# Kernel tuning notes

Measured on AMD Instinct MI355X. Metric: run time of the kernel, lower is better.

Reference implementation:

```python
import jax, jax.numpy as jnp
import numpy as np

B, DIN, E, FACTOR, STEPS, NH = 2048, 1024, 1024, 16, 3, 8
DH = E // NH
EPS = 1e-5


def layernorm(x, g, b):
    m = x.mean(-1, keepdims=True)
    v = ((x - m) ** 2).mean(-1, keepdims=True)
    return (x - m) / jnp.sqrt(v + EPS) * g + b


def setup_inputs() -> dict:
    key = jax.random.key(0)
    ks = iter(jax.random.split(key, 32))
    r = lambda shape, s=0.02: jax.random.normal(next(ks), shape, dtype=jnp.float32) * s
    F = E * FACTOR
    return {
        "image_feat": jax.random.normal(next(ks), (B, DIN), dtype=jnp.float32),
        "text_feat": jax.random.normal(next(ks), (B, DIN), dtype=jnp.float32),
        # fusion block
        "fc1_w": r((F, DIN)), "fc1_b": jnp.zeros((F,), jnp.float32),
        "fc2_w": r((F, DIN)), "fc2_b": jnp.zeros((F,), jnp.float32),
        "fc3_w": r((E, F)), "fc3_b": jnp.zeros((E,), jnp.float32),
        "ln_g": jnp.ones((E,), jnp.float32), "ln_b": jnp.zeros((E,), jnp.float32),
        # per-step MHA + FFN + norms, stacked over STEPS
        "Wqkv": r((STEPS, 3 * E, E)), "bqkv": jnp.zeros((STEPS, 3 * E), jnp.float32),
        "Wo": r((STEPS, E, E)), "bo": jnp.zeros((STEPS, E), jnp.float32),
        "W1": r((STEPS, E, E)), "b1": jnp.zeros((STEPS, E), jnp.float32),
        "W2": r((STEPS, E, E)), "b2": jnp.zeros((STEPS, E), jnp.float32),
        "n1_g": jnp.ones((STEPS, E), jnp.float32), "n1_b": jnp.zeros((STEPS, E), jnp.float32),
        "n2_g": jnp.ones((STEPS, E), jnp.float32), "n2_b": jnp.zeros((STEPS, E), jnp.float32),
        # output projection
        "Wout": r((DIN, E)), "bout": jnp.zeros((DIN,), jnp.float32),
    }


def mha_step(q, ctx, Wqkv, bqkv, Wo, bo):
    # q: [B,E] (query len 1), ctx: [B,L,E]
    Wq, Wk, Wv = Wqkv[:E], Wqkv[E:2 * E], Wqkv[2 * E:]
    bq, bk, bv = bqkv[:E], bqkv[E:2 * E], bqkv[2 * E:]
    L = ctx.shape[1]
    qh = (q @ Wq.T + bq).reshape(B, NH, DH)
    kh = (ctx @ Wk.T + bk).reshape(B, L, NH, DH)
    vh = (ctx @ Wv.T + bv).reshape(B, L, NH, DH)
    scores = jnp.einsum("bhd,blhd->bhl", qh, kh) / jnp.sqrt(jnp.float32(DH))
    attn = jax.nn.softmax(scores, axis=-1)
    out = jnp.einsum("bhl,blhd->bhd", attn, vh).reshape(B, E)
    return out @ Wo.T + bo


def reference(image_feat, text_feat, fc1_w, fc1_b, fc2_w, fc2_b, fc3_w, fc3_b,
              ln_g, ln_b, Wqkv, bqkv, Wo, bo, W1, b1, W2, b2,
              n1_g, n1_b, n2_g, n2_b, Wout, bout):
    # fusion block (dropout = identity in eval)
    fused = (image_feat @ fc1_w.T + fc1_b) * (text_feat @ fc2_w.T + fc2_b)
    fused = layernorm(fused @ fc3_w.T + fc3_b, ln_g, ln_b)  # [B,E]
    ctx = fused[:, None, :]  # [B,1,E]
    x = fused
    for i in range(STEPS):
        attn = mha_step(x, ctx, Wqkv[i], bqkv[i], Wo[i], bo[i])
        x = x + layernorm(attn, n1_g[i], n1_b[i])
        ffn = jax.nn.relu(x @ W1[i].T + b1[i]) @ W2[i].T + b2[i]
        x = x + layernorm(ffn, n2_g[i], n2_b[i])
        ctx = jnp.concatenate([ctx, x[:, None, :]], axis=1)
    final_output = x @ Wout.T + bout  # [B,DIN]
    return final_output, ctx
```

## Files before the change

### kernel.cpp

```cpp
#include <hip/hip_runtime.h>

#define TB 256

typedef __attribute__((ext_vector_type(8))) short short8;
typedef __attribute__((ext_vector_type(4))) float f32x4;
typedef unsigned short u16;

constexpr int B_  = 2048;
constexpr int DIN = 1024;
constexpr int E   = 1024;
constexpr int F   = 16384;
constexpr int E3  = 3072;
constexpr int CH  = 4096;
constexpr int FH  = 8192;

__device__ __forceinline__ u16 f2bf(float f) {
  union { float f; unsigned u; } v; v.f = f;
  unsigned r = v.u + 0x7fffu + ((v.u >> 16) & 1u);
  return (u16)(r >> 16);
}
__device__ __forceinline__ float bf2f(u16 u) {
  union { unsigned u; float f; } v; v.u = ((unsigned)u) << 16;
  return v.f;
}

__device__ __forceinline__ void gload16(const void* g, void* l) {
  __builtin_amdgcn_global_load_lds(
      (const __attribute__((address_space(1))) void*)g,
      (__attribute__((address_space(3))) void*)l, 16, 0, 0);
}

__device__ __forceinline__ void tile_xy(int& tx, int& ty) {
  int gx = gridDim.x;
  int nwg = gx * gridDim.y;
  int wg = blockIdx.y * gx + blockIdx.x;
  if ((nwg & 7) == 0) wg = (wg & 7) * (nwg >> 3) + (wg >> 3);
  tx = wg % gx; ty = wg / gx;
}

__device__ __forceinline__ int swz16(int o) {
  return o ^ (((o >> 7) & 7) << 4);
}

__global__ __launch_bounds__(256) void cvt_kernel(const float* __restrict__ s,
                                                  u16* __restrict__ d, int n) {
  int i = (blockIdx.x * 256 + threadIdx.x) * 4;
  if (i >= n) return;
  float4 v = *(const float4*)&s[i];
  ushort4 o;
  o.x = f2bf(v.x); o.y = f2bf(v.y); o.z = f2bf(v.z); o.w = f2bf(v.w);
  *(ushort4*)&d[i] = o;
}

__global__ __launch_bounds__(256) void fill_kernel(float* p, int n, float v) {
  int i = blockIdx.x * 256 + threadIdx.x;
  if (i < n) p[i] = v;
}

__global__ __launch_bounds__(256) void relu_bias_cvt_kernel(
    const float* __restrict__ hF, const float* __restrict__ bias,
    u16* __restrict__ out) {
  size_t i = ((size_t)blockIdx.x * 256 + threadIdx.x) * 4;
  int col = (int)(i & 1023);
  float4 v = *(const float4*)&hF[i];
  float4 b = *(const float4*)&bias[col];
  ushort4 o;
  float x0 = v.x + b.x, x1 = v.y + b.y, x2 = v.z + b.z, x3 = v.w + b.w;
  o.x = f2bf(x0 > 0.f ? x0 : 0.f);
  o.y = f2bf(x1 > 0.f ? x1 : 0.f);
  o.z = f2bf(x2 > 0.f ? x2 : 0.f);
  o.w = f2bf(x3 > 0.f ? x3 : 0.f);
  *(ushort4*)&out[i] = o;
}

__global__ __launch_bounds__(256) void bias_add_kernel(
    float* __restrict__ out, const float* __restrict__ bias) {
  size_t i = ((size_t)blockIdx.x * 256 + threadIdx.x) * 4;
  int col = (int)(i & 1023);
  float4 v = *(const float4*)&out[i];
  float4 b = *(const float4*)&bias[col];
  v.x += b.x; v.y += b.y; v.z += b.z; v.w += b.w;
  *(float4*)&out[i] = v;
}

template <int EPI>
__global__ __launch_bounds__(512, 2) void gemm256(
    const u16* __restrict__ A, int sA,
    const u16* __restrict__ Bw, int sB,
    const float* __restrict__ bias, const u16* __restrict__ gate,
    void* __restrict__ Out, int ldOut, int ksz) {
  __shared__ __align__(16) char smem[131072];
  const int tid = threadIdx.x, lane = tid & 63, w = tid >> 6;
  const int wm = w >> 2, wn = w & 3;
  int tx, ty; tile_xy(tx, ty);
  const int m0 = tx * 256, n0 = ty * 256;
  const int k0 = blockIdx.z * ksz;
  const int nt = ksz >> 6;
  const int lr = lane & 15;

  f32x4 acc[8][4] = {};

  auto stage = [&](const u16* __restrict__ G, int gs, int gr0, int kk, int tb, int j) {
    int P = j * 8192 + w * 1024 + lane * 16;
    int L = swz16(P);
    int row = L >> 7, colb = L & 127;
    gload16(G + (size_t)(gr0 + row) * gs + kk + (colb >> 1),
            &smem[tb + j * 8192 + w * 1024]);
  };
  auto rdA = [&](int tb, int mf, int kh) -> short8 {
    int Lo = (wm * 128 + mf * 16 + lr) * 128 + kh * 64 + (lane >> 4) * 16;
    return *(const short8*)&smem[tb + swz16(Lo)];
  };
  auto rdB = [&](int tb, int nf, int kh) -> short8 {
    int Lo = (wn * 64 + nf * 16 + lr) * 128 + kh * 64 + (lane >> 4) * 16;
    return *(const short8*)&smem[tb + swz16(Lo)];
  };

#pragma unroll
  for (int j = 0; j < 4; ++j) stage(A, sA, m0, k0, 0, j);
#pragma unroll
  for (int j = 0; j < 4; ++j) stage(Bw, sB, n0, k0, 65536, j);
  if (nt > 1) {
#pragma unroll
    for (int j = 0; j < 4; ++j) stage(Bw, sB, n0, k0 + 64, 65536 + 32768, j);
    asm volatile("s_waitcnt vmcnt(4)" ::: "memory");
  } else {
    asm volatile("s_waitcnt vmcnt(0)" ::: "memory");
  }
  __builtin_amdgcn_sched_barrier(0);
  __builtin_amdgcn_s_barrier();

  for (int t = 0; t < nt; ++t) {
    const int sa = (t & 1) * 32768;
    const int sb = 65536 + (t & 1) * 32768;
    short8 bfr[4][2], afr[2][2];
#pragma unroll
    for (int nf = 0; nf < 4; ++nf)
#pragma unroll
      for (int kh = 0; kh < 2; ++kh) bfr[nf][kh] = rdB(sb, nf, kh);
#pragma unroll
    for (int mf = 0; mf < 2; ++mf)
#pragma unroll
      for (int kh = 0; kh < 2; ++kh) afr[mf][kh] = rdA(sa, mf, kh);
    if (t + 1 < nt) {
      const int s2 = ((t + 1) & 1) * 32768;
#pragma unroll
      for (int j = 0; j < 4; ++j) stage(A, sA, m0, k0 + (t + 1) * 64, s2, j);
    }
    __builtin_amdgcn_sched_barrier(0);
    __builtin_amdgcn_s_barrier();
    __builtin_amdgcn_s_setprio(1);
#pragma unroll
    for (int mf = 0; mf < 2; ++mf)
#pragma unroll
      for (int nf = 0; nf < 4; ++nf)
#pragma unroll
        for (int kh = 0; kh < 2; ++kh)
          acc[mf][nf] = __builtin_amdgcn_mfma_f32_16x16x32_bf16(
              afr[mf][kh], bfr[nf][kh], acc[mf][nf], 0, 0, 0);
    __builtin_amdgcn_s_setprio(0);
    __builtin_amdgcn_sched_barrier(0);
    __builtin_amdgcn_s_barrier();
#pragma unroll
    for (int q = 1; q < 4; ++q) {
#pragma unroll
      for (int mf = 0; mf < 2; ++mf)
#pragma unroll
        for (int kh = 0; kh < 2; ++kh) afr[mf][kh] = rdA(sa, q * 2 + mf, kh);
      if (q < 3) {
        if (t + 2 < nt) {
#pragma unroll
          for (int j = 0; j < 2; ++j)
            stage(Bw, sB, n0, k0 + (t + 2) * 64, sb, (q - 1) * 2 + j);
        }
      } else {
        if (t + 2 < nt)      asm volatile("s_waitcnt vmcnt(4)" ::: "memory");
        else if (t + 1 < nt) asm volatile("s_waitcnt vmcnt(0)" ::: "memory");
      }
      __builtin_amdgcn_sched_barrier(0);
      __builtin_amdgcn_s_barrier();
      __builtin_amdgcn_s_setprio(1);
#pragma unroll
      for (int mf = 0; mf < 2; ++mf)
#pragma unroll
        for (int nf = 0; nf < 4; ++nf)
#pragma unroll
          for (int kh = 0; kh < 2; ++kh)
            acc[q * 2 + mf][nf] = __builtin_amdgcn_mfma_f32_16x16x32_bf16(
                afr[mf][kh], bfr[nf][kh], acc[q * 2 + mf][nf], 0, 0, 0);
      __builtin_amdgcn_s_setprio(0);
      __builtin_amdgcn_sched_barrier(0);
      __builtin_amdgcn_s_barrier();
    }
  }

  const int rb = (lane >> 4) * 4;
#pragma unroll
  for (int mf = 0; mf < 8; ++mf) {
#pragma unroll
    for (int nf = 0; nf < 4; ++nf) {
      int row0 = m0 + wm * 128 + mf * 16 + rb;
      int col  = n0 + wn * 64 + nf * 16 + lr;
      float bv = (EPI == 3 || bias == nullptr) ? 0.f : bias[col];
#pragma unroll
      for (int r = 0; r < 4; ++r) {
        float v = acc[mf][nf][r] + bv;
        size_t idx = (size_t)(row0 + r) * ldOut + col;
        if (EPI == 1)      ((u16*)Out)[idx] = f2bf(v);
        else if (EPI == 3) atomicAdd((float*)Out + idx, v);
        else if (EPI == 4) ((u16*)Out)[idx] = f2bf(v * bf2f(gate[idx]));
        else               ((float*)Out)[idx] = v;
      }
    }
  }
}

template <int EPI>
__global__ __launch_bounds__(TB) void gemm_bt(
    const u16* __restrict__ A, int sA,
    const u16* __restrict__ Bw, int sB,
    const float* __restrict__ bias, const u16* __restrict__ gate,
    void* __restrict__ Out, int ldOut, int Kext, int ksz) {
  __shared__ u16 As[128 * 32];
  __shared__ u16 Bs[128 * 32];
  const int tid = threadIdx.x, lane = tid & 63, w = tid >> 6;
  const int wr = w >> 1, wc = w & 1;
  int tx, ty; tile_xy(tx, ty);
  const int m0 = tx * 128, n0 = ty * 128;
  const int k0 = blockIdx.z * ksz;
  const int kend = min(k0 + ksz, Kext);

  f32x4 acc[4][4] = {};
  const int lr = lane & 15, lk = (lane >> 4) * 8;

  for (int kk = k0; kk < kend; kk += 32) {
#pragma unroll
    for (int is = 0; is < 2; ++is) {
      int c = is * 256 + tid;
      int r = c >> 2, kc = (c & 3) << 3;
      size_t lb = (size_t)(is * 256 + w * 64) * 8;
      gload16(A  + (size_t)(m0 + r) * sA + kk + kc, &As[lb]);
      gload16(Bw + (size_t)(n0 + r) * sB + kk + kc, &Bs[lb]);
    }
    __syncthreads();
    short8 af[4], bfv[4];
#pragma unroll
    for (int m = 0; m < 4; ++m)
      af[m] = *(const short8*)&As[(wr * 64 + m * 16 + lr) * 32 + lk];
#pragma unroll
    for (int n = 0; n < 4; ++n)
      bfv[n] = *(const short8*)&Bs[(wc * 64 + n * 16 + lr) * 32 + lk];
#pragma unroll
    for (int m = 0; m < 4; ++m)
#pragma unroll
      for (int n = 0; n < 4; ++n)
        acc[m][n] = __builtin_amdgcn_mfma_f32_16x16x32_bf16(af[m], bfv[n], acc[m][n], 0, 0, 0);
    __syncthreads();
  }

  const int rbase = (lane >> 4) * 4;
#pragma unroll
  for (int m = 0; m < 4; ++m) {
#pragma unroll
    for (int n = 0; n < 4; ++n) {
      int row0 = m0 + wr * 64 + m * 16 + rbase;
      int col  = n0 + wc * 64 + n * 16 + lr;
      float bv = (EPI == 3 || bias == nullptr) ? 0.f : bias[col];
#pragma unroll
      for (int r = 0; r < 4; ++r) {
        float v = acc[m][n][r] + bv;
        size_t idx = (size_t)(row0 + r) * ldOut + col;
        if (EPI == 0)      ((float*)Out)[idx] = v;
        else if (EPI == 1) ((u16*)Out)[idx] = f2bf(v);
        else if (EPI == 2) ((u16*)Out)[idx] = f2bf(v > 0.f ? v : 0.f);
        else if (EPI == 3) atomicAdd((float*)Out + idx, v);
        else               ((u16*)Out)[idx] = f2bf(v * bf2f(gate[idx]));
      }
    }
  }
}

template <int EPI>
__global__ __launch_bounds__(TB) void gemm_wf32(
    const u16* __restrict__ A, int sA,
    const float* __restrict__ Bw, int sB,
    const float* __restrict__ bias, void* __restrict__ Out, int ldOut,
    int Kext, int ksz) {
  __shared__ u16 As[128 * 32];
  __shared__ u16 Bs[128 * 32];
  const int tid = threadIdx.x, lane = tid & 63, w = tid >> 6;
  const int wr = w >> 1, wc = w & 1;
  int tx, ty; tile_xy(tx, ty);
  const int m0 = tx * 128, n0 = ty * 128;
  const int k0 = blockIdx.z * ksz;
  const int kend = min(k0 + ksz, Kext);

  f32x4 acc[4][4] = {};
  const int lr = lane & 15, lk = (lane >> 4) * 8;

  for (int kk = k0; kk < kend; kk += 32) {
#pragma unroll
    for (int is = 0; is < 2; ++is) {
      int c = is * 256 + tid;
      int r = c >> 2, kc = (c & 3) << 3;
      gload16(A + (size_t)(m0 + r) * sA + kk + kc,
              &As[(size_t)(is * 256 + w * 64) * 8]);
    }
#pragma unroll
    for (int p = 0; p < 4; ++p) {
      int t = tid + p * 256;
      int r = t >> 3, c4 = (t & 7) << 2;
      float4 v = *(const float4*)&Bw[(size_t)(n0 + r) * sB + kk + c4];
      ushort4 o;
      o.x = f2bf(v.x); o.y = f2bf(v.y); o.z = f2bf(v.z); o.w = f2bf(v.w);
      *(ushort4*)&Bs[r * 32 + c4] = o;
    }
    __syncthreads();
    short8 af[4], bfv[4];
#pragma unroll
    for (int m = 0; m < 4; ++m)
      af[m] = *(const short8*)&As[(wr * 64 + m * 16 + lr) * 32 + lk];
#pragma unroll
    for (int n = 0; n < 4; ++n)
      bfv[n] = *(const short8*)&Bs[(wc * 64 + n * 16 + lr) * 32 + lk];
#pragma unroll
    for (int m = 0; m < 4; ++m)
#pragma unroll
      for (int n = 0; n < 4; ++n)
        acc[m][n] = __builtin_amdgcn_mfma_f32_16x16x32_bf16(af[m], bfv[n], acc[m][n], 0, 0, 0);
    __syncthreads();
  }

  const int rbase = (lane >> 4) * 4;
#pragma unroll
  for (int m = 0; m < 4; ++m) {
#pragma unroll
    for (int n = 0; n < 4; ++n) {
      int row0 = m0 + wr * 64 + m * 16 + rbase;
      int col  = n0 + wc * 64 + n * 16 + lr;
      float bv = (EPI == 3 || bias == nullptr) ? 0.f : bias[col];
#pragma unroll
      for (int r = 0; r < 4; ++r) {
        float v = acc[m][n][r] + bv;
        size_t idx = (size_t)(row0 + r) * ldOut + col;
        if (EPI == 0)      ((float*)Out)[idx] = v;
        else if (EPI == 1) ((u16*)Out)[idx] = f2bf(v);
        else if (EPI == 2) ((u16*)Out)[idx] = f2bf(v > 0.f ? v : 0.f);
        else               atomicAdd((float*)Out + idx, v);
      }
    }
  }
}

__global__ __launch_bounds__(TB) void gemm_dual_wf32(
    const u16* __restrict__ A1, const u16* __restrict__ A2, int sA,
    const float* __restrict__ B1, const float* __restrict__ B2, int sB,
    const float* __restrict__ bias1, const float* __restrict__ bias2,
    u16* __restrict__ Out, int ldOut, int K) {
  __shared__ u16 As1[128 * 32];
  __shared__ u16 As2[128 * 32];
  __shared__ u16 Bs1[128 * 32];
  __shared__ u16 Bs2[128 * 32];
  const int tid = threadIdx.x, lane = tid & 63, w = tid >> 6;
  const int wr = w >> 1, wc = w & 1;
  int tx, ty; tile_xy(tx, ty);
  const int m0 = tx * 128, n0 = ty * 128;

  f32x4 acc1[4][4] = {};
  f32x4 acc2[4][4] = {};
  const int lr = lane & 15, lk = (lane >> 4) * 8;

  for (int kk = 0; kk < K; kk += 32) {
#pragma unroll
    for (int is = 0; is < 2; ++is) {
      int c = is * 256 + tid;
      int r = c >> 2, kc = (c & 3) << 3;
      size_t lb = (size_t)(is * 256 + w * 64) * 8;
      gload16(A1 + (size_t)(m0 + r) * sA + kk + kc, &As1[lb]);
      gload16(A2 + (size_t)(m0 + r) * sA + kk + kc, &As2[lb]);
    }
#pragma unroll
    for (int p = 0; p < 4; ++p) {
      int t = tid + p * 256;
      int r = t >> 3, c4 = (t & 7) << 2;
      float4 v1 = *(const float4*)&B1[(size_t)(n0 + r) * sB + kk + c4];
      float4 v2 = *(const float4*)&B2[(size_t)(n0 + r) * sB + kk + c4];
      ushort4 o1, o2;
      o1.x = f2bf(v1.x); o1.y = f2bf(v1.y); o1.z = f2bf(v1.z); o1.w = f2bf(v1.w);
      o2.x = f2bf(v2.x); o2.y = f2bf(v2.y); o2.z = f2bf(v2.z); o2.w = f2bf(v2.w);
      *(ushort4*)&Bs1[r * 32 + c4] = o1;
      *(ushort4*)&Bs2[r * 32 + c4] = o2;
    }
    __syncthreads();
    short8 a1[4], a2[4], b1v[4], b2v[4];
#pragma unroll
    for (int m = 0; m < 4; ++m) {
      a1[m] = *(const short8*)&As1[(wr * 64 + m * 16 + lr) * 32 + lk];
      a2[m] = *(const short8*)&As2[(wr * 64 + m * 16 + lr) * 32 + lk];
    }
#pragma unroll
    for (int n = 0; n < 4; ++n) {
      b1v[n] = *(const short8*)&Bs1[(wc * 64 + n * 16 + lr) * 32 + lk];
      b2v[n] = *(const short8*)&Bs2[(wc * 64 + n * 16 + lr) * 32 + lk];
    }
#pragma unroll
    for (int m = 0; m < 4; ++m)
#pragma unroll
      for (int n = 0; n < 4; ++n) {
        acc1[m][n] = __builtin_amdgcn_mfma_f32_16x16x32_bf16(a1[m], b1v[n], acc1[m][n], 0, 0, 0);
        acc2[m][n] = __builtin_amdgcn_mfma_f32_16x16x32_bf16(a2[m], b2v[n], acc2[m][n], 0, 0, 0);
      }
    __syncthreads();
  }

  const int rbase = (lane >> 4) * 4;
#pragma unroll
  for (int m = 0; m < 4; ++m) {
#pragma unroll
    for (int n = 0; n < 4; ++n) {
      int row0 = m0 + wr * 64 + m * 16 + rbase;
      int col  = n0 + wc * 64 + n * 16 + lr;
      float bv1 = bias1[col], bv2 = bias2[col];
#pragma unroll
      for (int r = 0; r < 4; ++r) {
        float v = (acc1[m][n][r] + bv1) * (acc2[m][n][r] + bv2);
        Out[(size_t)(row0 + r) * ldOut + col] = f2bf(v);
      }
    }
  }
}

template <int MODE>
__global__ __launch_bounds__(256) void resln_kernel(
    const float* __restrict__ Y, const float* __restrict__ preb,
    const float* __restrict__ g, const float* __restrict__ bp,
    float* __restrict__ x, u16* __restrict__ xb,
    float* __restrict__ ctxo, int ctxRow) {
  const int r = blockIdx.x, tid = threadIdx.x;
  const size_t base = (size_t)r * 1024 + tid * 4;
  float4 y4 = *(const float4*)&Y[base];
  float y[4] = {y4.x, y4.y, y4.z, y4.w};
  if (preb != nullptr) {
    float4 p4 = *(const float4*)&preb[tid * 4];
    y[0] += p4.x; y[1] += p4.y; y[2] += p4.z; y[3] += p4.w;
  }
  float s = y[0] + y[1] + y[2] + y[3];
  float q = y[0] * y[0] + y[1] * y[1] + y[2] * y[2] + y[3] * y[3];
  __shared__ float red[8];
  for (int o = 32; o; o >>= 1) { s += __shfl_xor(s, o); q += __shfl_xor(q, o); }
  int wv = tid >> 6;
  if ((tid & 63) == 0) { red[wv] = s; red[4 + wv] = q; }
  __syncthreads();
  s = red[0] + red[1] + red[2] + red[3];
  q = red[4] + red[5] + red[6] + red[7];
  float mean = s * (1.f / 1024.f);
  float var  = q * (1.f / 1024.f) - mean * mean;
  float rs   = rsqrtf(var + 1e-5f);
  float4 g4 = *(const float4*)&g[tid * 4];
  float4 b4 = *(const float4*)&bp[tid * 4];
  float gg[4] = {g4.x, g4.y, g4.z, g4.w};
  float bb[4] = {b4.x, b4.y, b4.z, b4.w};
  float xv[4];
#pragma unroll
  for (int j = 0; j < 4; ++j) {
    float val = (y[j] - mean) * rs * gg[j] + bb[j];
    xv[j] = (MODE == 0) ? val : x[base + j] + val;
  }
  *(float4*)&x[base] = make_float4(xv[0], xv[1], xv[2], xv[3]);
  ushort4 xo;
  xo.x = f2bf(xv[0]); xo.y = f2bf(xv[1]); xo.z = f2bf(xv[2]); xo.w = f2bf(xv[3]);
  *(ushort4*)&xb[base] = xo;
  if (MODE != 1) {
    size_t cb = ((size_t)r * 4 + ctxRow) * 1024 + tid * 4;
    *(float4*)&ctxo[cb] = make_float4(xv[0], xv[1], xv[2], xv[3]);
  }
}

__global__ __launch_bounds__(64) void attn_kernel(const u16* __restrict__ qkv,
                                                  u16* __restrict__ out, int L) {
  const int b = blockIdx.x >> 3, h = blockIdx.x & 7;
  const int lane = threadIdx.x;
  const size_t qoff = ((size_t)(L - 1) * B_ + b) * E3 + h * 128;
  float q0 = bf2f(qkv[qoff + lane]);
  float q1 = bf2f(qkv[qoff + 64 + lane]);
  float sc[3];
  for (int l = 0; l < L; ++l) {
    size_t kb = ((size_t)l * B_ + b) * E3 + 1024 + h * 128;
    float p = q0 * bf2f(qkv[kb + lane]) + q1 * bf2f(qkv[kb + 64 + lane]);
    for (int o = 32; o; o >>= 1) p += __shfl_xor(p, o);
    sc[l] = p * 0.08838834764831843f;
  }
  float m = sc[0];
  for (int l = 1; l < L; ++l) m = fmaxf(m, sc[l]);
  float wsum = 0.f, wgt[3];
  for (int l = 0; l < L; ++l) { wgt[l] = expf(sc[l] - m); wsum += wgt[l]; }
  float inv = 1.f / wsum;
  float o0 = 0.f, o1 = 0.f;
  for (int l = 0; l < L; ++l) {
    size_t vb = ((size_t)l * B_ + b) * E3 + 2048 + h * 128;
    o0 += wgt[l] * bf2f(qkv[vb + lane]);
    o1 += wgt[l] * bf2f(qkv[vb + 64 + lane]);
  }
  out[(size_t)b * 1024 + h * 128 + lane]      = f2bf(o0 * inv);
  out[(size_t)b * 1024 + h * 128 + 64 + lane] = f2bf(o1 * inv);
}

extern "C" void kernel_launch(void* const* d_in, const int* in_sizes, int n_in,
                              void* d_out, int out_size, void* d_ws, size_t ws_size,
                              hipStream_t stream) {
  (void)in_sizes; (void)n_in;
  const float* image = (const float*)d_in[0];
  const float* text  = (const float*)d_in[1];
  const float* fc1_w = (const float*)d_in[2];
  const float* fc1_b = (const float*)d_in[3];
  const float* fc2_w = (const float*)d_in[4];
  const float* fc2_b = (const float*)d_in[5];
  const float* fc3_w = (const float*)d_in[6];
  const float* fc3_b = (const float*)d_in[7];
  const float* ln_g  = (const float*)d_in[8];
  const float* ln_b  = (const float*)d_in[9];
  const float* Wqkv  = (const float*)d_in[10];
  const float* bqkv  = (const float*)d_in[11];
  const float* Wo    = (const float*)d_in[12];
  const float* bo    = (const float*)d_in[13];
  const float* W1    = (const float*)d_in[14];
  const float* b1    = (const float*)d_in[15];
  const float* W2    = (const float*)d_in[16];
  const float* b2    = (const float*)d_in[17];
  const float* n1_g  = (const float*)d_in[18];
  const float* n1_b  = (const float*)d_in[19];
  const float* n2_g  = (const float*)d_in[20];
  const float* n2_b  = (const float*)d_in[21];
  const float* WoutW = (const float*)d_in[22];
  const float* boutW = (const float*)d_in[23];

  float* outF   = (float*)d_out;
  float* ctxOut = outF + (size_t)B_ * DIN;
  char* ws = (char*)d_ws;

  auto cvt = [&](const float* s, u16* d, size_t n) {
    cvt_kernel<<<dim3((unsigned)((n + 1023) / 1024)), 256, 0, stream>>>(s, d, (int)n);
  };

  const size_t NEED_A = 232783872;
  if (ws_size >= NEED_A) {
    size_t off = 0;
    auto carve = [&](size_t bytes) -> char* {
      char* p = ws + off; off += (bytes + 255) & ~(size_t)255; return p;
    };
    u16* imgB  = (u16*)carve((size_t)B_ * DIN * 2);
    u16* txtB  = (u16*)carve((size_t)B_ * DIN * 2);
    u16* fc1B  = (u16*)carve((size_t)F * DIN * 2);
    u16* fc2B  = (u16*)carve((size_t)F * DIN * 2);
    u16* fc3B  = (u16*)carve((size_t)E * F * 2);
    u16* WqkvB = (u16*)carve((size_t)3 * E3 * E * 2);
    u16* WoB   = (u16*)carve((size_t)3 * E * E * 2);
    u16* W1B   = (u16*)carve((size_t)3 * E * E * 2);
    u16* W2B   = (u16*)carve((size_t)3 * E * E * 2);
    u16* WoutB = (u16*)carve((size_t)DIN * E * 2);
    char* U    = carve((size_t)B_ * F * 2);
    float* xF  = (float*)carve((size_t)B_ * E * 4);
    float* hF  = (float*)carve((size_t)B_ * E * 4);
    u16* g1B    = (u16*)U;
    u16* fusedC = (u16*)(U + (size_t)B_ * FH * 2);
    u16* qkvB   = (u16*)(U);
    u16* ctxB   = (u16*)(U + 37748736);
    u16* attnB  = (u16*)(U + 37748736 + 16777216);
    u16* h1B    = (u16*)(U + 37748736 + 16777216 + 4194304);
    u16* xbB    = (u16*)(U + 37748736 + 16777216 + 8388608);

    cvt(image, imgB, (size_t)B_ * DIN);
    cvt(text,  txtB, (size_t)B_ * DIN);
    cvt(fc1_w, fc1B, (size_t)F * DIN);
    cvt(fc2_w, fc2B, (size_t)F * DIN);
    cvt(fc3_w, fc3B, (size_t)E * F);
    cvt(Wqkv,  WqkvB, (size_t)3 * E3 * E);
    cvt(Wo,    WoB,   (size_t)3 * E * E);
    cvt(W1,    W1B,   (size_t)3 * E * E);
    cvt(W2,    W2B,   (size_t)3 * E * E);
    cvt(WoutW, WoutB, (size_t)DIN * E);
    hipMemsetAsync(hF, 0, (size_t)B_ * E * 4, stream);

    for (int c = 0; c < 2; ++c) {
      gemm256<1><<<dim3(B_ / 256, FH / 256), 512, 0, stream>>>(
          imgB, DIN, fc1B + (size_t)c * FH * DIN, DIN,
          fc1_b + (size_t)c * FH, nullptr, g1B, FH, DIN);
      gemm256<4><<<dim3(B_ / 256, FH / 256), 512, 0, stream>>>(
          txtB, DIN, fc2B + (size_t)c * FH * DIN, DIN,
          fc2_b + (size_t)c * FH, g1B, fusedC, FH, DIN);
      gemm256<3><<<dim3(B_ / 256, E / 256, 8), 512, 0, stream>>>(
          fusedC, FH, fc3B + (size_t)c * FH, F, nullptr, nullptr, hF, E, FH / 8);
    }

    resln_kernel<0><<<B_, 256, 0, stream>>>(hF, fc3_b, ln_g, ln_b, xF, ctxB, ctxOut, 0);

    for (int i = 0; i < 3; ++i) {
      int L = i + 1;
      gemm256<1><<<dim3(L * B_ / 256, E3 / 256), 512, 0, stream>>>(
          ctxB, E, WqkvB + (size_t)i * E3 * E, E, bqkv + (size_t)i * E3, nullptr,
          qkvB, E3, E);
      attn_kernel<<<B_ * 8, 64, 0, stream>>>(qkvB, attnB, L);
      hipMemsetAsync(hF, 0, (size_t)B_ * E * 4, stream);
      gemm_bt<3><<<dim3(B_ / 128, E / 128, 2), TB, 0, stream>>>(
          attnB, E, WoB + (size_t)i * E * E, E, nullptr, nullptr, hF, E, E, E / 2);
      resln_kernel<1><<<B_, 256, 0, stream>>>(
          hF, bo + (size_t)i * E, n1_g + (size_t)i * E, n1_b + (size_t)i * E,
          xF, xbB, nullptr, 0);
      hipMemsetAsync(hF, 0, (size_t)B_ * E * 4, stream);
      gemm_bt<3><<<dim3(B_ / 128, E / 128, 2), TB, 0, stream>>>(
          xbB, E, W1B + (size_t)i * E * E, E, nullptr, nullptr, hF, E, E, E / 2);
      relu_bias_cvt_kernel<<<B_ * E / 1024, 256, 0, stream>>>(
          hF, b1 + (size_t)i * E, h1B);
      hipMemsetAsync(hF, 0, (size_t)B_ * E * 4, stream);
      gemm_bt<3><<<dim3(B_ / 128, E / 128, 2), TB, 0, stream>>>(
          h1B, E, W2B + (size_t)i * E * E, E, nullptr, nullptr, hF, E, E, E / 2);
      resln_kernel<2><<<B_, 256, 0, stream>>>(
          hF, b2 + (size_t)i * E, n2_g + (size_t)i * E, n2_b + (size_t)i * E,
          xF, ctxB + (size_t)(i + 1) * B_ * E, ctxOut, i + 1);
    }

    hipMemsetAsync(outF, 0, (size_t)B_ * DIN * 4, stream);
    gemm_bt<3><<<dim3(B_ / 128, DIN / 128, 2), TB, 0, stream>>>(
        ctxB + (size_t)3 * B_ * E, E, WoutB, E, nullptr, nullptr, outF, DIN, E, E / 2);
    bias_add_kernel<<<B_ * DIN / 1024, 256, 0, stream>>>(outF, boutW);
    return;
  }

  size_t off = 0;
  auto carve = [&](size_t bytes) -> char* {
    char* p = ws + off; off += (bytes + 255) & ~(size_t)255; return p;
  };
  u16* imgB   = (u16*)carve((size_t)B_ * DIN * 2);
  u16* txtB   = (u16*)carve((size_t)B_ * DIN * 2);
  u16* fusedC = (u16*)carve((size_t)B_ * CH * 2);
  u16* qkvB   = (u16*)carve((size_t)3 * B_ * E3 * 2);
  u16* ctxB   = (u16*)carve((size_t)4 * B_ * E * 2);
  u16* attnB  = (u16*)carve((size_t)B_ * E * 2);
  u16* h1B    = (u16*)carve((size_t)B_ * E * 2);
  u16* xbB    = (u16*)carve((size_t)B_ * E * 2);
  float* xF   = (float*)carve((size_t)B_ * E * 4);
  float* hF   = (float*)carve((size_t)B_ * E * 4);

  if (off > ws_size) {
    fill_kernel<<<(out_size + 255) / 256, 256, 0, stream>>>(outF, out_size, 12345.0f);
    return;
  }

  cvt(image, imgB, (size_t)B_ * DIN);
  cvt(text,  txtB, (size_t)B_ * DIN);
  hipMemsetAsync(hF, 0, (size_t)B_ * E * 4, stream);

  for (int c = 0; c < F / CH; ++c) {
    gemm_dual_wf32<<<dim3(B_ / 128, CH / 128), TB, 0, stream>>>(
        imgB, txtB, DIN,
        fc1_w + (size_t)c * CH * DIN, fc2_w + (size_t)c * CH * DIN, DIN,
        fc1_b + (size_t)c * CH, fc2_b + (size_t)c * CH, fusedC, CH, DIN);
    gemm_wf32<3><<<dim3(B_ / 128, E / 128, 2), TB, 0, stream>>>(
        fusedC, CH, fc3_w + (size_t)c * CH, F, nullptr, hF, E, CH, CH / 2);
  }
  resln_kernel<0><<<B_, 256, 0, stream>>>(hF, fc3_b, ln_g, ln_b, xF, ctxB, ctxOut, 0);

  for (int i = 0; i < 3; ++i) {
    int L = i + 1;
    gemm_wf32<1><<<dim3(L * B_ / 128, E3 / 128), TB, 0, stream>>>(
        ctxB, E, Wqkv + (size_t)i * E3 * E, E, bqkv + (size_t)i * E3, qkvB, E3, E, E);
    attn_kernel<<<B_ * 8, 64, 0, stream>>>(qkvB, attnB, L);
    gemm_wf32<0><<<dim3(B_ / 128, E / 128), TB, 0, stream>>>(
        attnB, E, Wo + (size_t)i * E * E, E, bo + (size_t)i * E, hF, E, E, E);
    resln_kernel<1><<<B_, 256, 0, stream>>>(
        hF, nullptr, n1_g + (size_t)i * E, n1_b + (size_t)i * E, xF, xbB, nullptr, 0);
    gemm_wf32<2><<<dim3(B_ / 128, E / 128), TB, 0, stream>>>(
        xbB, E, W1 + (size_t)i * E * E, E, b1 + (size_t)i * E, h1B, E, E, E);
    gemm_wf32<0><<<dim3(B_ / 128, E / 128), TB, 0, stream>>>(
        h1B, E, W2 + (size_t)i * E * E, E, b2 + (size_t)i * E, hF, E, E, E);
    resln_kernel<2><<<B_, 256, 0, stream>>>(
        hF, nullptr, n2_g + (size_t)i * E, n2_b + (size_t)i * E, xF,
        ctxB + (size_t)(i + 1) * B_ * E, ctxOut, i + 1);
  }
  gemm_wf32<0><<<dim3(B_ / 128, DIN / 128), TB, 0, stream>>>(
      ctxB + (size_t)3 * B_ * E, E, WoutW, E, boutW, outF, DIN, E, E);
}
```

Baseline: 956.9 us.

## Simplify GEMM main loop to whole-tile double buffering with one barrier

Replaces the four-phase GEMM K-loop with a simple double buffer. Previously B tiles were prefetched two steps ahead and A one step ahead, with a block barrier around each of four MFMA sub-phases. Now the whole next A and B tile is issued at the start of each iteration, and the MFMAs run in two halves of four row fragments each. There is a single vmcnt(0) wait and one barrier per iteration. This is meant to cut barrier and wait overhead, at the cost of less interleaving of global loads and LDS reads with MFMA work and more register pressure from larger fragment arrays.

New measurement: 950.3 us. Within noise of the previous version (-0.7%).

```diff
diff --git a/kernel.cpp b/kernel.cpp
--- a/kernel.cpp
+++ b/kernel.cpp
@@ -120,38 +120,34 @@
   for (int j = 0; j < 4; ++j) stage(A, sA, m0, k0, 0, j);
 #pragma unroll
   for (int j = 0; j < 4; ++j) stage(Bw, sB, n0, k0, 65536, j);
-  if (nt > 1) {
-#pragma unroll
-    for (int j = 0; j < 4; ++j) stage(Bw, sB, n0, k0 + 64, 65536 + 32768, j);
-    asm volatile("s_waitcnt vmcnt(4)" ::: "memory");
-  } else {
-    asm volatile("s_waitcnt vmcnt(0)" ::: "memory");
-  }
+  asm volatile("s_waitcnt vmcnt(0)" ::: "memory");
   __builtin_amdgcn_sched_barrier(0);
   __builtin_amdgcn_s_barrier();
 
+  int cur = 0;
   for (int t = 0; t < nt; ++t) {
-    const int sa = (t & 1) * 32768;
-    const int sb = 65536 + (t & 1) * 32768;
-    short8 bfr[4][2], afr[2][2];
+    const int sa = cur * 32768;
+    const int sb = 65536 + cur * 32768;
+    if (t + 1 < nt) {
+      const int sa2 = (cur ^ 1) * 32768;
+      const int sb2 = 65536 + (cur ^ 1) * 32768;
+#pragma unroll
+      for (int j = 0; j < 4; ++j) stage(A, sA, m0, k0 + (t + 1) * 64, sa2, j);
+#pragma unroll
+      for (int j = 0; j < 4; ++j) stage(Bw, sB, n0, k0 + (t + 1) * 64, sb2, j);
+    }
+    short8 bfr[4][2], afr[4][2];
 #pragma unroll
     for (int nf = 0; nf < 4; ++nf)
 #pragma unroll
       for (int kh = 0; kh < 2; ++kh) bfr[nf][kh] = rdB(sb, nf, kh);
 #pragma unroll
-    for (int mf = 0; mf < 2; ++mf)
+    for (int mf = 0; mf < 4; ++mf)
 #pragma unroll
       for (int kh = 0; kh < 2; ++kh) afr[mf][kh] = rdA(sa, mf, kh);
-    if (t + 1 < nt) {
-      const int s2 = ((t + 1) & 1) * 32768;
-#pragma unroll
-      for (int j = 0; j < 4; ++j) stage(A, sA, m0, k0 + (t + 1) * 64, s2, j);
-    }
-    __builtin_amdgcn_sched_barrier(0);
-    __builtin_amdgcn_s_barrier();
     __builtin_amdgcn_s_setprio(1);
 #pragma unroll
-    for (int mf = 0; mf < 2; ++mf)
+    for (int mf = 0; mf < 4; ++mf)
 #pragma unroll
       for (int nf = 0; nf < 4; ++nf)
 #pragma unroll
@@ -159,39 +155,26 @@
           acc[mf][nf] = __builtin_amdgcn_mfma_f32_16x16x32_bf16(
               afr[mf][kh], bfr[nf][kh], acc[mf][nf], 0, 0, 0);
     __builtin_amdgcn_s_setprio(0);
-    __builtin_amdgcn_sched_barrier(0);
-    __builtin_amdgcn_s_barrier();
-#pragma unroll
-    for (int q = 1; q < 4; ++q) {
-#pragma unroll
-      for (int mf = 0; mf < 2; ++mf)
-#pragma unroll
-        for (int kh = 0; kh < 2; ++kh) afr[mf][kh] = rdA(sa, q * 2 + mf, kh);
-      if (q < 3) {
-        if (t + 2 < nt) {
-#pragma unroll
-          for (int j = 0; j < 2; ++j)
-            stage(Bw, sB, n0, k0 + (t + 2) * 64, sb, (q - 1) * 2 + j);
-        }
-      } else {
-        if (t + 2 < nt)      asm volatile("s_waitcnt vmcnt(4)" ::: "memory");
-        else if (t + 1 < nt) asm volatile("s_waitcnt vmcnt(0)" ::: "memory");
-      }
+#pragma unroll
+    for (int mf = 0; mf < 4; ++mf)
+#pragma unroll
+      for (int kh = 0; kh < 2; ++kh) afr[mf][kh] = rdA(sa, 4 + mf, kh);
+    __builtin_amdgcn_s_setprio(1);
+#pragma unroll
+    for (int mf = 0; mf < 4; ++mf)
+#pragma unroll
+      for (int nf = 0; nf < 4; ++nf)
+#pragma unroll
+        for (int kh = 0; kh < 2; ++kh)
+          acc[4 + mf][nf] = __builtin_amdgcn_mfma_f32_16x16x32_bf16(
+              afr[mf][kh], bfr[nf][kh], acc[4 + mf][nf], 0, 0, 0);
+    __builtin_amdgcn_s_setprio(0);
+    if (t + 1 < nt) {
+      asm volatile("s_waitcnt vmcnt(0)" ::: "memory");
       __builtin_amdgcn_sched_barrier(0);
       __builtin_amdgcn_s_barrier();
-      __builtin_amdgcn_s_setprio(1);
-#pragma unroll
-      for (int mf = 0; mf < 2; ++mf)
-#pragma unroll
-        for (int nf = 0; nf < 4; ++nf)
-#pragma unroll
-          for (int kh = 0; kh < 2; ++kh)
-            acc[q * 2 + mf][nf] = __builtin_amdgcn_mfma_f32_16x16x32_bf16(
-                afr[mf][kh], bfr[nf][kh], acc[q * 2 + mf][nf], 0, 0, 0);
-      __builtin_amdgcn_s_setprio(0);
-      __builtin_amdgcn_sched_barrier(0);
-      __builtin_amdgcn_s_barrier();
-    }
+    }
+    cur ^= 1;
   }
 
   const int rb = (lane >> 4) * 4;
```
